# Kernel optimization log

Measured on AMD Instinct MI355X. Metric: run time of the kernel, lower is better.

## Reference

```python
import jax, jax.numpy as jnp
import numpy as np

N_NODES = 50000
N_EDGES = 800000
INPUT_DIM = 8
HIDDEN_DIM = 128


def setup_inputs() -> dict:
    key = jax.random.key(0)
    k = jax.random.split(key, 8)
    x = jax.random.normal(k[0], (N_NODES, INPUT_DIM), dtype=jnp.float32)
    edge_index = jax.random.randint(k[1], (2, N_EDGES), 0, N_NODES, dtype=jnp.int64)
    edge_attr = jax.random.uniform(k[2], (N_EDGES, 1), dtype=jnp.float32)
    node_embedding = jax.random.normal(k[3], (N_NODES, HIDDEN_DIM), dtype=jnp.float32)
    # Linear weights stored as [in, out] so y = x @ W (bias=False everywhere)
    s1 = 1.0 / np.sqrt(INPUT_DIM)
    sh = 1.0 / np.sqrt(HIDDEN_DIM)
    W1 = jax.random.uniform(k[4], (INPUT_DIM, HIDDEN_DIM), jnp.float32, -s1, s1)
    W2 = jax.random.uniform(k[5], (HIDDEN_DIM, HIDDEN_DIM), jnp.float32, -sh, sh)
    W3 = jax.random.uniform(k[6], (HIDDEN_DIM, HIDDEN_DIM), jnp.float32, -sh, sh)
    W4 = jax.random.uniform(k[7], (1, HIDDEN_DIM), jnp.float32, -1.0, 1.0)
    return {"x": x, "edge_index": edge_index, "edge_attr": edge_attr,
            "node_embedding": node_embedding, "W1": W1, "W2": W2, "W3": W3, "W4": W4}


def reference(x, edge_index, edge_attr, node_embedding, W1, W2, W3, W4):
    n = x.shape[0]
    row, col = edge_index[0], edge_index[1]
    # theta_1(x): [N, hidden]
    node_feature_embedding = x @ W1
    # gather neighbor embeddings along edges, scatter-sum to destination rows
    node_embedding_aggr = jax.ops.segment_sum(node_embedding[col], row, num_segments=n)
    # relu(theta_4(edge_attr)): [E, hidden], then scatter-sum to rows
    edge_feature_embedding = jax.nn.relu(edge_attr @ W4)
    edge_embedding_aggr = jax.ops.segment_sum(edge_feature_embedding, row, num_segments=n)
    return jax.nn.relu(node_feature_embedding + node_embedding_aggr @ W2 + edge_embedding_aggr @ W3)
```

## Files before the change

kernel.cpp:

```cpp
#include <hip/hip_runtime.h>

#define N_NODES 50000
#define N_EDGES 800000
#define IN_DIM  8
#define HD      128
#define N_SCAN_BLOCKS ((N_NODES + 255) / 256)
#define NREP 16
#define NTILES ((N_NODES + 63) / 64)
#define N_HIST_BLOCKS (N_EDGES / 256)
#define NRANGE 8
#define RANGE_N (N_NODES / NRANGE)
#define N_HISTB (NREP * NRANGE)
#define GRID_P1 (N_HISTB + 2)
#define GRID_SG (N_SCAN_BLOCKS + NTILES)

typedef unsigned short ushort_t;
typedef unsigned int uint_t;
typedef __attribute__((ext_vector_type(8))) short short8;
typedef __attribute__((ext_vector_type(4))) float float4v;
typedef __attribute__((ext_vector_type(4))) int int4v;
typedef __attribute__((ext_vector_type(2))) uint_t uint2v;

static __device__ inline unsigned short f2bf(float f) {
    unsigned u = __float_as_uint(f);
    unsigned r = (u + 0x7FFF + ((u >> 16) & 1)) >> 16;
    return (unsigned short)r;
}
static __device__ inline float bf2f(unsigned short b) {
    return __uint_as_float(((unsigned)b) << 16);
}

__global__ __launch_bounds__(256, 2)
void phase1_kernel(const short8* ,
                   const float* __restrict__ W2,
                   short8* __restrict__ blob,
                   const int* __restrict__ ei,
                   int* __restrict__ cnt,
                   ushort_t* __restrict__ rank16,
                   const float* __restrict__ W4,
                   const float* __restrict__ W3,
                   float* __restrict__ v3,
                   int* __restrict__ bsums) {
    __shared__ uint_t hcnt[RANGE_N];
    int t = threadIdx.x;

    if (blockIdx.x < N_HISTB) {
        int rep   = blockIdx.x & (NREP - 1);
        int range = blockIdx.x / NREP;
        int rbase = range * RANGE_N;
        for (int i = t; i < RANGE_N; i += 256) hcnt[i] = 0u;
        __syncthreads();
        int g    = t >> 6;
        int lane = t & 63;
        int NC = (N_HIST_BLOCKS - rep + NREP - 1) / NREP;
        int j = g;
        int4v rv = {0, 0, 0, 0};
        if (j < NC)
            rv = *(const int4v*)(ei + (rep + j * NREP) * 256 + lane * 4);
        while (j < NC) {
            int jn = j + 4;
            int4v nx = {0, 0, 0, 0};
            if (jn < NC)
                nx = *(const int4v*)(ei + (rep + jn * NREP) * 256 + lane * 4);
            int e0 = (rep + j * NREP) * 256 + lane * 4;
#pragma unroll
            for (int q = 0; q < 4; ++q) {
                int lr = rv[q] - rbase;
                if ((unsigned)lr < (unsigned)RANGE_N) {
                    uint_t rk = atomicAdd(&hcnt[lr], 1u);
                    rank16[e0 + q] = (ushort_t)rk;
                }
            }
            rv = nx; j = jn;
        }
        __syncthreads();
        int* crow = cnt + rep * N_NODES + rbase;
        for (int i = t; i < RANGE_N; i += 256) crow[i] = (int)hcnt[i];
        return;
    }

    if (blockIdx.x == N_HISTB) {
#pragma unroll
        for (int i = 0; i < 8; ++i) {
            int slot = t * 8 + i;
            int f    = slot >> 6;
            int lane = slot & 63;
            int ct = f >> 2, ki = f & 3;
            int n16 = lane & 15, quad = lane >> 4;
            short8 fr;
#pragma unroll
            for (int jj = 0; jj < 8; ++jj) {
                int k = ki * 32 + quad * 8 + jj;
                fr[jj] = (short)f2bf(W2[k * HD + ct * 16 + n16]);
            }
            blob[slot] = fr;
        }
        return;
    }

    bsums[t] = 0;
    if (t < HD) {
        float acc = 0.f;
        for (int k = 0; k < HD; ++k) {
            float w = W4[k];
            w = w > 0.f ? w : 0.f;
            acc += w * W3[k * HD + t];
        }
        v3[t] = acc;
    }
}

__global__ __launch_bounds__(256, 2)
void scan_gemm_kernel(const int* __restrict__ cnt,
                      int* __restrict__ off,
                      int* __restrict__ bases,
                      int* __restrict__ bsums,
                      const float* __restrict__ emb,
                      const short8* __restrict__ blob,
                      ushort_t* __restrict__ T16) {
    __shared__ int lds[256];
    int t = threadIdx.x;

    if (blockIdx.x < N_SCAN_BLOCKS) {
        int n = blockIdx.x * 256 + t;
        int c[NREP];
        int tsum = 0;
#pragma unroll
        for (int r = 0; r < NREP; ++r) {
            c[r] = (n < N_NODES) ? cnt[r * N_NODES + n] : 0;
            tsum += c[r];
        }
        lds[t] = tsum;
        __syncthreads();
        for (int o = 1; o < 256; o <<= 1) {
            int add = (t >= o) ? lds[t - o] : 0;
            __syncthreads();
            lds[t] += add;
            __syncthreads();
        }
        int ex = lds[t] - tsum;
        int total = lds[255];
        if (n < N_NODES) {
            off[n] = ex;
            int run = ex;
#pragma unroll
            for (int r = 0; r < NREP; ++r) {
                bases[r * N_NODES + n] = run;
                run += c[r];
            }
        }
        for (int bb = blockIdx.x + 1 + t; bb < N_SCAN_BLOCKS; bb += 256)
            atomicAdd(&bsums[bb], total);
        return;
    }

    int tt   = blockIdx.x - N_SCAN_BLOCKS;
    int wave = t >> 6;
    int lane = t & 63;
    int n16  = lane & 15;
    int quad = lane >> 4;

    short8 wfrag[8][4];
#pragma unroll
    for (int ct = 0; ct < 8; ++ct)
#pragma unroll
        for (int ki = 0; ki < 4; ++ki)
            wfrag[ct][ki] = blob[(ct * 4 + ki) * 64 + lane];

    int rowbase = tt * 64 + wave * 16;
    int row  = rowbase + n16;
    int rowc = row < N_NODES ? row : N_NODES - 1;
    const float4v* arow = (const float4v*)(emb + (size_t)rowc * HD);

    short8 efrag[4];
#pragma unroll
    for (int ki = 0; ki < 4; ++ki) {
        float4v lo = __builtin_nontemporal_load(&arow[ki * 8 + quad * 2]);
        float4v hi = __builtin_nontemporal_load(&arow[ki * 8 + quad * 2 + 1]);
        short8 a;
        a[0] = (short)f2bf(lo[0]); a[1] = (short)f2bf(lo[1]);
        a[2] = (short)f2bf(lo[2]); a[3] = (short)f2bf(lo[3]);
        a[4] = (short)f2bf(hi[0]); a[5] = (short)f2bf(hi[1]);
        a[6] = (short)f2bf(hi[2]); a[7] = (short)f2bf(hi[3]);
        efrag[ki] = a;
    }

    float4v acc[8];
#pragma unroll
    for (int ct = 0; ct < 8; ++ct) acc[ct] = (float4v){0.f, 0.f, 0.f, 0.f};

#pragma unroll
    for (int ki = 0; ki < 4; ++ki)
#pragma unroll
        for (int ct = 0; ct < 8; ++ct)
            acc[ct] = __builtin_amdgcn_mfma_f32_16x16x32_bf16(
                wfrag[ct][ki], efrag[ki], acc[ct], 0, 0, 0);

    if (row < N_NODES) {
        ushort_t* dstu = T16 + (size_t)row * HD + quad * 4;
#pragma unroll
        for (int ct = 0; ct < 8; ++ct) {
            uint2v v;
            v[0] = (uint_t)f2bf(acc[ct][0]) | ((uint_t)f2bf(acc[ct][1]) << 16);
            v[1] = (uint_t)f2bf(acc[ct][2]) | ((uint_t)f2bf(acc[ct][3]) << 16);
            *(uint2v*)(dstu + ct * 16) = v;
        }
    }
}

__global__ void fill_kernel(const int* __restrict__ ei,
                            const float* __restrict__ attr,
                            const ushort_t* __restrict__ rank16,
                            const int* __restrict__ bases,
                            const int* __restrict__ bsums,
                            uint_t* __restrict__ packed) {
    int e = blockIdx.x * 256 + threadIdx.x;
    int rep = (e >> 8) & (NREP - 1);
    int r = ei[e];
    int pos = bases[rep * N_NODES + r] + bsums[r >> 8] + (int)rank16[e];
    uint_t p = ((uint_t)f2bf(attr[e]) << 16) | (uint_t)ei[N_EDGES + e];
    packed[pos] = p;
}

__global__ void aggregate_kernel(const int* __restrict__ off,
                                 const int* __restrict__ bsums,
                                 const uint_t* __restrict__ packed,
                                 const ushort_t* __restrict__ T16,
                                 const float* __restrict__ x,
                                 const float* __restrict__ W1,
                                 const float* __restrict__ v3,
                                 float* __restrict__ out) {
    int tid  = blockIdx.x * 256 + threadIdx.x;
    int node = tid >> 4;
    int lane = tid & 15;
    int s  = off[node] + bsums[node >> 8];
    int e1 = (node + 1 == N_NODES) ? N_EDGES
                                   : off[node + 1] + bsums[(node + 1) >> 8];
    int deg = e1 - s;

    float acc[8];
#pragma unroll
    for (int i = 0; i < 8; ++i) acc[i] = 0.f;
    float ssum = 0.f;

    for (int base = 0; base < deg; base += 16) {
        int rem = deg - base; if (rem > 16) rem = 16;
        uint_t p = 0;
        if (lane < rem) p = __builtin_nontemporal_load(&packed[s + base + lane]);
        ssum += __uint_as_float(p & 0xFFFF0000u);
        int col = (int)(p & 0xFFFFu);
        int j = 0;
        for (; j + 4 <= rem; j += 4) {
            int c0 = __shfl(col, j + 0, 16);
            int c1 = __shfl(col, j + 1, 16);
            int c2 = __shfl(col, j + 2, 16);
            int c3 = __shfl(col, j + 3, 16);
            short8 t0 = ((const short8*)(T16 + (size_t)c0 * HD))[lane];
            short8 t1 = ((const short8*)(T16 + (size_t)c1 * HD))[lane];
            short8 t2 = ((const short8*)(T16 + (size_t)c2 * HD))[lane];
            short8 t3 = ((const short8*)(T16 + (size_t)c3 * HD))[lane];
#pragma unroll
            for (int i = 0; i < 8; ++i)
                acc[i] += (bf2f((ushort_t)t0[i]) + bf2f((ushort_t)t1[i]))
                        + (bf2f((ushort_t)t2[i]) + bf2f((ushort_t)t3[i]));
        }
        for (; j < rem; ++j) {
            int c = __shfl(col, j, 16);
            short8 tv = ((const short8*)(T16 + (size_t)c * HD))[lane];
#pragma unroll
            for (int i = 0; i < 8; ++i)
                acc[i] += bf2f((ushort_t)tv[i]);
        }
    }
    for (int o = 8; o; o >>= 1) ssum += __shfl_xor(ssum, o, 16);

    const float4v* v3p = (const float4v*)v3;
    float4v b0 = v3p[lane * 2], b1 = v3p[lane * 2 + 1];
    acc[0] += ssum * b0[0]; acc[1] += ssum * b0[1];
    acc[2] += ssum * b0[2]; acc[3] += ssum * b0[3];
    acc[4] += ssum * b1[0]; acc[5] += ssum * b1[1];
    acc[6] += ssum * b1[2]; acc[7] += ssum * b1[3];
#pragma unroll
    for (int i = 0; i < IN_DIM; ++i) {
        float xi = x[node * IN_DIM + i];
        const float4v* wp = (const float4v*)(W1 + i * HD);
        float4v w0 = wp[lane * 2], w1 = wp[lane * 2 + 1];
        acc[0] += xi * w0[0]; acc[1] += xi * w0[1];
        acc[2] += xi * w0[2]; acc[3] += xi * w0[3];
        acc[4] += xi * w1[0]; acc[5] += xi * w1[1];
        acc[6] += xi * w1[2]; acc[7] += xi * w1[3];
    }
    float4v o0, o1;
    o0[0] = fmaxf(acc[0], 0.f); o0[1] = fmaxf(acc[1], 0.f);
    o0[2] = fmaxf(acc[2], 0.f); o0[3] = fmaxf(acc[3], 0.f);
    o1[0] = fmaxf(acc[4], 0.f); o1[1] = fmaxf(acc[5], 0.f);
    o1[2] = fmaxf(acc[6], 0.f); o1[3] = fmaxf(acc[7], 0.f);
    float4v* op = (float4v*)(out + (size_t)node * HD);
    __builtin_nontemporal_store(o0, op + lane * 2);
    __builtin_nontemporal_store(o1, op + lane * 2 + 1);
}

extern "C" void kernel_launch(void* const* d_in, const int* in_sizes, int n_in,
                              void* d_out, int out_size, void* d_ws, size_t ws_size,
                              hipStream_t stream) {
    const float* x    = (const float*)d_in[0];
    const int*   ei   = (const int*)  d_in[1];
    const float* attr = (const float*)d_in[2];
    const float* emb  = (const float*)d_in[3];
    const float* W1   = (const float*)d_in[4];
    const float* W2   = (const float*)d_in[5];
    const float* W3   = (const float*)d_in[6];
    const float* W4   = (const float*)d_in[7];
    float* out = (float*)d_out;

    char* w = (char*)d_ws;
    uint_t*   packed = (uint_t*)w;
    ushort_t* T16    = (ushort_t*)(w + (size_t)N_EDGES * 4);
    short8*   blob   = (short8*)((char*)T16 + (size_t)N_NODES * HD * 2);
    int*      off    = (int*)((char*)blob + 2048 * 16);
    int*      bases  = off + N_NODES + 4;
    int*      cnt    = bases + NREP * N_NODES;
    int*      bsums  = cnt + NREP * N_NODES;
    float*    v3     = (float*)(bsums + 256);
    ushort_t* rank16 = (ushort_t*)(v3 + HD);

    phase1_kernel<<<GRID_P1, 256, 0, stream>>>(
        (const short8*)blob, W2, blob, ei, cnt, rank16, W4, W3, v3, bsums);
    scan_gemm_kernel<<<GRID_SG, 256, 0, stream>>>(
        cnt, off, bases, bsums, emb, blob, T16);
    fill_kernel  <<<N_HIST_BLOCKS, 256, 0, stream>>>(ei, attr, rank16, bases, bsums, packed);
    aggregate_kernel<<<(N_NODES * 16) / 256, 256, 0, stream>>>(
        off, bsums, packed, T16, x, W1, v3, out);
}
```

Measured before the change: 188.5 us.

## Move embedding GEMM into histogram kernel and convert W2 inline

Moves the node_embedding×W2 MFMA GEMM tiles out of the scan kernel and into the first kernel, so they run alongside the histogram blocks. Each tile now reads W2 in fp32 and converts it to bf16 itself, which removes the separate weight-packing blob step. The scan becomes its own small kernel. The histogram range count is doubled, which halves the LDS histogram per block. The trade-off is redundant W2 loads and conversions in every GEMM tile and two extra kernel-boundary dependencies, in exchange for overlapping the GEMM with the histogram.

Measured after the change: 174.7 us. -7.3%, faster.

```diff
diff --git a/kernel.cpp b/kernel.cpp
--- a/kernel.cpp
+++ b/kernel.cpp
@@ -4,15 +4,14 @@
 #define N_EDGES 800000
 #define IN_DIM  8
 #define HD      128
-#define N_SCAN_BLOCKS ((N_NODES + 255) / 256)
 #define NREP 16
-#define NTILES ((N_NODES + 63) / 64)
-#define N_HIST_BLOCKS (N_EDGES / 256)
-#define NRANGE 8
+#define NRANGE 16
 #define RANGE_N (N_NODES / NRANGE)
 #define N_HISTB (NREP * NRANGE)
-#define GRID_P1 (N_HISTB + 2)
-#define GRID_SG (N_SCAN_BLOCKS + NTILES)
+#define N_HIST_BLOCKS (N_EDGES / 256)
+#define NTILES ((N_NODES + 63) / 64)
+#define N_SCAN_BLOCKS ((N_NODES + 255) / 256)
+#define GRID_P1 (N_HISTB + NTILES + 1)
 
 typedef unsigned short ushort_t;
 typedef unsigned int uint_t;
@@ -31,9 +30,9 @@
 }
 
 __global__ __launch_bounds__(256, 2)
-void phase1_kernel(const short8* ,
+void phase1_kernel(const float* __restrict__ emb,
                    const float* __restrict__ W2,
-                   short8* __restrict__ blob,
+                   ushort_t* __restrict__ T16,
                    const int* __restrict__ ei,
                    int* __restrict__ cnt,
                    ushort_t* __restrict__ rank16,
@@ -50,8 +49,7 @@
         int rbase = range * RANGE_N;
         for (int i = t; i < RANGE_N; i += 256) hcnt[i] = 0u;
         __syncthreads();
-        int g    = t >> 6;
-        int lane = t & 63;
+        int g = t >> 6, lane = t & 63;
         int NC = (N_HIST_BLOCKS - rep + NREP - 1) / NREP;
         int j = g;
         int4v rv = {0, 0, 0, 0};
@@ -79,93 +77,25 @@
         return;
     }
 
-    if (blockIdx.x == N_HISTB) {
-#pragma unroll
-        for (int i = 0; i < 8; ++i) {
-            int slot = t * 8 + i;
-            int f    = slot >> 6;
-            int lane = slot & 63;
-            int ct = f >> 2, ki = f & 3;
-            int n16 = lane & 15, quad = lane >> 4;
-            short8 fr;
-#pragma unroll
-            for (int jj = 0; jj < 8; ++jj) {
-                int k = ki * 32 + quad * 8 + jj;
-                fr[jj] = (short)f2bf(W2[k * HD + ct * 16 + n16]);
+    if (blockIdx.x == N_HISTB + NTILES) {
+        bsums[t] = 0;
+        if (t < HD) {
+            float acc = 0.f;
+            for (int k = 0; k < HD; ++k) {
+                float w = W4[k];
+                w = w > 0.f ? w : 0.f;
+                acc += w * W3[k * HD + t];
             }
-            blob[slot] = fr;
+            v3[t] = acc;
         }
         return;
     }
 
-    bsums[t] = 0;
-    if (t < HD) {
-        float acc = 0.f;
-        for (int k = 0; k < HD; ++k) {
-            float w = W4[k];
-            w = w > 0.f ? w : 0.f;
-            acc += w * W3[k * HD + t];
-        }
-        v3[t] = acc;
-    }
-}
-
-__global__ __launch_bounds__(256, 2)
-void scan_gemm_kernel(const int* __restrict__ cnt,
-                      int* __restrict__ off,
-                      int* __restrict__ bases,
-                      int* __restrict__ bsums,
-                      const float* __restrict__ emb,
-                      const short8* __restrict__ blob,
-                      ushort_t* __restrict__ T16) {
-    __shared__ int lds[256];
-    int t = threadIdx.x;
-
-    if (blockIdx.x < N_SCAN_BLOCKS) {
-        int n = blockIdx.x * 256 + t;
-        int c[NREP];
-        int tsum = 0;
-#pragma unroll
-        for (int r = 0; r < NREP; ++r) {
-            c[r] = (n < N_NODES) ? cnt[r * N_NODES + n] : 0;
-            tsum += c[r];
-        }
-        lds[t] = tsum;
-        __syncthreads();
-        for (int o = 1; o < 256; o <<= 1) {
-            int add = (t >= o) ? lds[t - o] : 0;
-            __syncthreads();
-            lds[t] += add;
-            __syncthreads();
-        }
-        int ex = lds[t] - tsum;
-        int total = lds[255];
-        if (n < N_NODES) {
-            off[n] = ex;
-            int run = ex;
-#pragma unroll
-            for (int r = 0; r < NREP; ++r) {
-                bases[r * N_NODES + n] = run;
-                run += c[r];
-            }
-        }
-        for (int bb = blockIdx.x + 1 + t; bb < N_SCAN_BLOCKS; bb += 256)
-            atomicAdd(&bsums[bb], total);
-        return;
-    }
-
-    int tt   = blockIdx.x - N_SCAN_BLOCKS;
+    int tt   = blockIdx.x - N_HISTB;
     int wave = t >> 6;
     int lane = t & 63;
     int n16  = lane & 15;
     int quad = lane >> 4;
-
-    short8 wfrag[8][4];
-#pragma unroll
-    for (int ct = 0; ct < 8; ++ct)
-#pragma unroll
-        for (int ki = 0; ki < 4; ++ki)
-            wfrag[ct][ki] = blob[(ct * 4 + ki) * 64 + lane];
 
     int rowbase = tt * 64 + wave * 16;
     int row  = rowbase + n16;
@@ -189,12 +119,21 @@
 #pragma unroll
     for (int ct = 0; ct < 8; ++ct) acc[ct] = (float4v){0.f, 0.f, 0.f, 0.f};
 
-#pragma unroll
-    for (int ki = 0; ki < 4; ++ki)
+    const float* wbase = W2 + (quad * 8) * HD + n16;
+#pragma unroll
+    for (int ki = 0; ki < 4; ++ki) {
+        const float* wk = wbase + ki * 32 * HD;
+        short8 wf[8];
+#pragma unroll
+        for (int ct = 0; ct < 8; ++ct)
+#pragma unroll
+            for (int j = 0; j < 8; ++j)
+                wf[ct][j] = (short)f2bf(wk[j * HD + ct * 16]);
 #pragma unroll
         for (int ct = 0; ct < 8; ++ct)
             acc[ct] = __builtin_amdgcn_mfma_f32_16x16x32_bf16(
-                wfrag[ct][ki], efrag[ki], acc[ct], 0, 0, 0);
+                wf[ct], efrag[ki], acc[ct], 0, 0, 0);
+    }
 
     if (row < N_NODES) {
         ushort_t* dstu = T16 + (size_t)row * HD + quad * 4;
@@ -206,6 +145,43 @@
             *(uint2v*)(dstu + ct * 16) = v;
         }
     }
+}
+
+__global__ void scan1_kernel(const int* __restrict__ cnt,
+                             int* __restrict__ off,
+                             int* __restrict__ bases,
+                             int* __restrict__ bsums) {
+    __shared__ int lds[256];
+    int t = threadIdx.x;
+    int n = blockIdx.x * 256 + t;
+    int c[NREP];
+    int tsum = 0;
+#pragma unroll
+    for (int r = 0; r < NREP; ++r) {
+        c[r] = (n < N_NODES) ? cnt[r * N_NODES + n] : 0;
+        tsum += c[r];
+    }
+    lds[t] = tsum;
+    __syncthreads();
+    for (int o = 1; o < 256; o <<= 1) {
+        int add = (t >= o) ? lds[t - o] : 0;
+        __syncthreads();
+        lds[t] += add;
+        __syncthreads();
+    }
+    int ex = lds[t] - tsum;
+    int total = lds[255];
+    if (n < N_NODES) {
+        off[n] = ex;
+        int run = ex;
+#pragma unroll
+        for (int r = 0; r < NREP; ++r) {
+            bases[r * N_NODES + n] = run;
+            run += c[r];
+        }
+    }
+    for (int bb = blockIdx.x + 1 + t; bb < N_SCAN_BLOCKS; bb += 256)
+        atomicAdd(&bsums[bb], total);
 }
 
 __global__ void fill_kernel(const int* __restrict__ ei,
@@ -316,8 +292,7 @@
     char* w = (char*)d_ws;
     uint_t*   packed = (uint_t*)w;
     ushort_t* T16    = (ushort_t*)(w + (size_t)N_EDGES * 4);
-    short8*   blob   = (short8*)((char*)T16 + (size_t)N_NODES * HD * 2);
-    int*      off    = (int*)((char*)blob + 2048 * 16);
+    int*      off    = (int*)((char*)T16 + (size_t)N_NODES * HD * 2);
     int*      bases  = off + N_NODES + 4;
     int*      cnt    = bases + NREP * N_NODES;
     int*      bsums  = cnt + NREP * N_NODES;
@@ -325,9 +300,8 @@
     ushort_t* rank16 = (ushort_t*)(v3 + HD);
 
     phase1_kernel<<<GRID_P1, 256, 0, stream>>>(
-        (const short8*)blob, W2, blob, ei, cnt, rank16, W4, W3, v3, bsums);
-    scan_gemm_kernel<<<GRID_SG, 256, 0, stream>>>(
-        cnt, off, bases, bsums, emb, blob, T16);
+        emb, W2, T16, ei, cnt, rank16, W4, W3, v3, bsums);
+    scan1_kernel <<<N_SCAN_BLOCKS, 256, 0, stream>>>(cnt, off, bases, bsums);
     fill_kernel  <<<N_HIST_BLOCKS, 256, 0, stream>>>(ei, attr, rank16, bases, bsums, packed);
     aggregate_kernel<<<(N_NODES * 16) / 256, 256, 0, stream>>>(
         off, bsums, packed, T16, x, W1, v3, out);
```
